# Performance work log

Measured on AMD Instinct MI355X. Metric: run time of the kernel, lower is better.

Reference implementation:

```python
import jax, jax.numpy as jnp
import numpy as np

EPS = 1e-12

def _prelu(x, a):
    return jnp.where(x >= 0, x, a * x)

def _l2norm(x):
    n = jnp.sqrt(jnp.sum(x * x, axis=1, keepdims=True))
    return x / jnp.maximum(n, EPS)

def setup_inputs() -> dict:
    key = jax.random.key(0)
    ks = jax.random.split(key, 8)
    N, E, F_IN, F_OUT = 262144, 4194304, 128, 64
    feat = jax.random.normal(ks[0], (N, F_IN), dtype=jnp.float32)
    edge_src = jax.random.randint(ks[1], (E,), 0, N, dtype=jnp.int32)
    edge_dst = jax.random.randint(ks[2], (E,), 0, N, dtype=jnp.int32)
    edge_w = jax.random.uniform(ks[3], (E,), dtype=jnp.float32)
    # Glorot-uniform projection weight, zero biases (reset_parameters)
    lim = float(np.sqrt(6.0 / (F_IN + F_OUT)))
    weight = jax.random.uniform(ks[4], (F_IN, F_OUT), minval=-lim, maxval=lim, dtype=jnp.float32)
    bias = jnp.zeros((F_OUT,), dtype=jnp.float32)
    prelu_a = jnp.full((1,), 0.25, dtype=jnp.float32)
    lim2 = float(np.sqrt(1.0 / F_OUT))  # torch Linear default init range
    w_sub = jax.random.uniform(ks[5], (F_OUT, F_OUT), minval=-lim2, maxval=lim2, dtype=jnp.float32)
    b_sub = jnp.zeros((F_OUT,), dtype=jnp.float32)
    w_gcn = jax.random.uniform(ks[6], (F_OUT, F_OUT), minval=-lim2, maxval=lim2, dtype=jnp.float32)
    b_gcn = jnp.zeros((F_OUT,), dtype=jnp.float32)
    return {"feat": feat, "edge_src": edge_src, "edge_dst": edge_dst, "edge_w": edge_w,
            "weight": weight, "bias": bias, "prelu_a": prelu_a,
            "w_sub": w_sub, "b_sub": b_sub, "w_gcn": w_gcn, "b_gcn": b_gcn}

def reference(feat, edge_src, edge_dst, edge_w, weight, bias, prelu_a,
              w_sub, b_sub, w_gcn, b_gcn):
    N = feat.shape[0]
    G = N // 4  # 4 nodes per subgraph, anchors at stride 4
    # anchor rows extracted, then zeroed in the feature matrix (in-place in torch)
    anchor_embs = feat[::4, :]
    feat_z = feat.at[::4, :].set(0.0)
    anchor_out = _prelu(anchor_embs @ weight + bias, prelu_a)
    # GraphConv(norm='none', weight=False, bias=False) with edge weights:
    # h[dst] = sum_e w_e * (feat_z @ W)[src_e]
    in_feat = feat_z @ weight                      # [N, F_OUT]
    msgs = in_feat[edge_src] * edge_w[:, None]     # [E, F_OUT]
    h = jax.ops.segment_sum(msgs, edge_dst, num_segments=N)
    h = _prelu(h + bias, prelu_a)
    # AvgPooling per graph (each graph has exactly 4 nodes)
    seg = jnp.arange(N, dtype=jnp.int32) // 4
    subgraph_pool_emb = jax.ops.segment_sum(h, seg, num_segments=G) / 4.0
    gcn_emb = h[::4, :]
    subgraph_pool_emb = subgraph_pool_emb @ w_sub.T + b_sub
    gcn_emb = gcn_emb @ w_gcn.T + b_gcn
    return (_l2norm(subgraph_pool_emb), _l2norm(anchor_out), _l2norm(gcn_emb))
```

## Files before the change

### kernel.cpp

```cpp
#include <hip/hip_runtime.h>
#include <hip/hip_fp16.h>

#define EPSN 1e-12f
#define NBC  256
#define RBF  1024
#define CHK  8192
#define NWGMAX 1024
#define PU   4
#define WQS  16384.0f

typedef _Float16 half8_t __attribute__((ext_vector_type(8)));
typedef float    f32x4  __attribute__((ext_vector_type(4)));

__device__ __forceinline__ float rdlane(float v, int k) {
    return __int_as_float(__builtin_amdgcn_readlane(__float_as_int(v), k));
}
__device__ __forceinline__ float preluf(float x, float a) {
    return x >= 0.0f ? x : a * x;
}

__device__ __forceinline__ void transform_body(
    const float* __restrict__ feat, const float* __restrict__ weight,
    const float* __restrict__ bias, const float* __restrict__ prelu_a,
    __half* __restrict__ in_feat, float* __restrict__ out_anchor,
    int N, int wid, int totalWaves)
{
    const int lane = threadIdx.x & 63;
    const int r    = lane & 15;
    const int g    = lane >> 4;
    const int nt4  = N >> 4;

    half8_t bfr[4][4];
    #pragma unroll
    for (int nt = 0; nt < 4; ++nt)
        #pragma unroll
        for (int kq = 0; kq < 4; ++kq)
            #pragma unroll
            for (int e = 0; e < 8; ++e)
                bfr[nt][kq][e] =
                    (_Float16)weight[(kq * 32 + g * 8 + e) * 64 + nt * 16 + r];

    float bj[4];
    #pragma unroll
    for (int nt = 0; nt < 4; ++nt) bj[nt] = bias[nt * 16 + r];
    const float a = prelu_a[0];

    for (int t = wid; t < nt4; t += totalWaves) {
        const int rb = t << 4;

        f32x4 acc[4];
        #pragma unroll
        for (int nt = 0; nt < 4; ++nt) acc[nt] = (f32x4){0.f, 0.f, 0.f, 0.f};

        const float* fr = feat + (size_t)(rb + r) * 128 + g * 8;
        #pragma unroll
        for (int kq = 0; kq < 4; ++kq) {
            const float4 f0 = *(const float4*)(fr + kq * 32);
            const float4 f1 = *(const float4*)(fr + kq * 32 + 4);
            half8_t af;
            af[0] = (_Float16)f0.x; af[1] = (_Float16)f0.y;
            af[2] = (_Float16)f0.z; af[3] = (_Float16)f0.w;
            af[4] = (_Float16)f1.x; af[5] = (_Float16)f1.y;
            af[6] = (_Float16)f1.z; af[7] = (_Float16)f1.w;
            #pragma unroll
            for (int nt = 0; nt < 4; ++nt)
                acc[nt] = __builtin_amdgcn_mfma_f32_16x16x32_f16(
                    af, bfr[nt][kq], acc[nt], 0, 0, 0);
        }

        const int row0 = rb + g * 4;
        float ss = 0.0f, y[4];
        #pragma unroll
        for (int nt = 0; nt < 4; ++nt) {
            y[nt] = preluf(acc[nt][0] + bj[nt], a);
            ss = fmaf(y[nt], y[nt], ss);
        }
        ss += __shfl_xor(ss, 1, 16);
        ss += __shfl_xor(ss, 2, 16);
        ss += __shfl_xor(ss, 4, 16);
        ss += __shfl_xor(ss, 8, 16);
        const float inv = 1.0f / fmaxf(sqrtf(ss), EPSN);
        #pragma unroll
        for (int nt = 0; nt < 4; ++nt)
            out_anchor[(size_t)(row0 >> 2) * 64 + nt * 16 + r] = y[nt] * inv;
        #pragma unroll
        for (int nt = 0; nt < 4; ++nt)
            in_feat[(size_t)row0 * 64 + nt * 16 + r] = __float2half(0.0f);
        #pragma unroll
        for (int reg = 1; reg < 4; ++reg)
            #pragma unroll
            for (int nt = 0; nt < 4; ++nt)
                in_feat[(size_t)(row0 + reg) * 64 + nt * 16 + r] =
                    __float2half(acc[nt][reg]);
    }
}

__global__ __launch_bounds__(256) void k_tc(
    const float* __restrict__ feat, const float* __restrict__ weight,
    const float* __restrict__ bias, const float* __restrict__ prelu_a,
    __half* __restrict__ in_feat, float* __restrict__ out_anchor, int N,
    int nwg, int twT,
    const int* __restrict__ esrc, const int* __restrict__ edst, int E,
    unsigned* __restrict__ C)
{
    __shared__ unsigned hist[NBC];
    const int t = threadIdx.x;
    if ((int)blockIdx.x >= nwg) {
        const int tIdx = (int)blockIdx.x - nwg;
        const int wid  = tIdx * 4 + (t >> 6);
        transform_body(feat, weight, bias, prelu_a, in_feat, out_anchor,
                       N, wid, twT);
        return;
    }
    const int blk = (int)blockIdx.x;
    hist[t] = 0;
    __syncthreads();
    const int base = blk * CHK;
    for (int r = 0; r < CHK / (16 * 256); ++r) {
        int d[16];
        #pragma unroll
        for (int i = 0; i < 16; ++i) {
            const int idx = base + (r * 16 + i) * 256 + t;
            d[i] = -1;
            if (idx < E) {
                const int s = esrc[idx];
                if ((s & 3) != 0) d[i] = edst[idx];
            }
        }
        #pragma unroll
        for (int i = 0; i < 16; ++i)
            if (d[i] >= 0) atomicAdd(&hist[((unsigned)d[i]) >> 10], 1u);
    }
    __syncthreads();
    C[(size_t)blk * NBC + t] = hist[t];
}

__global__ __launch_bounds__(256) void s_scanA(
    unsigned* __restrict__ C, unsigned* __restrict__ T, int nwg)
{
    __shared__ unsigned ssum[256];
    const int i = blockIdx.x;
    const int t = threadIdx.x;
    const int PER = (nwg + 255) / 256;
    unsigned vals[4];
    unsigned run = 0;
    for (int p = 0; p < PER; ++p) {
        const int blk = t * PER + p;
        const unsigned v = (blk < nwg) ? C[(size_t)blk * NBC + i] : 0u;
        vals[p] = run;
        run += v;
    }
    ssum[t] = run;
    __syncthreads();
    for (int off = 1; off < 256; off <<= 1) {
        unsigned x = (t >= off) ? ssum[t - off] : 0u;
        __syncthreads();
        ssum[t] += x;
        __syncthreads();
    }
    const unsigned texcl = ssum[t] - run;
    for (int p = 0; p < PER; ++p) {
        const int blk = t * PER + p;
        if (blk < nwg) C[(size_t)blk * NBC + i] = texcl + vals[p];
    }
    if (t == 255) T[i] = ssum[255];
}

__global__ __launch_bounds__(1024) void s_scatter4(
    const int* __restrict__ esrc, const int* __restrict__ edst,
    const float* __restrict__ ew, int E,
    const unsigned* __restrict__ C, const unsigned* __restrict__ T, int nwg,
    uint2* __restrict__ recs)
{
    __shared__ uint2    buf[CHK];
    __shared__ unsigned cur[NBC];
    __shared__ unsigned cb [NBC];
    __shared__ unsigned ssum[NBC];
    const int blk = blockIdx.x;
    const int t   = threadIdx.x;

    unsigned Tt = 0, own = 0, nxt = 0;
    if (t < NBC) {
        Tt  = T[t];
        own = C[(size_t)blk * NBC + t];
        nxt = (blk + 1 < nwg) ? C[(size_t)(blk + 1) * NBC + t] : Tt;
        ssum[t] = Tt;
    }
    __syncthreads();
    for (int off = 1; off < NBC; off <<= 1) {
        unsigned x = 0;
        if (t < NBC && t >= off) x = ssum[t - off];
        __syncthreads();
        if (t < NBC) ssum[t] += x;
        __syncthreads();
    }
    const unsigned basepl = (t < NBC) ? (ssum[t] - Tt) : 0u;
    __syncthreads();

    const unsigned myc = nxt - own;
    if (t < NBC) ssum[t] = myc;
    __syncthreads();
    for (int off = 1; off < NBC; off <<= 1) {
        unsigned x = 0;
        if (t < NBC && t >= off) x = ssum[t - off];
        __syncthreads();
        if (t < NBC) ssum[t] += x;
        __syncthreads();
    }
    if (t < NBC) {
        const unsigned excl = ssum[t] - myc;
        cur[t] = excl;
        cb[t]  = basepl + own - excl;
    }
    __syncthreads();
    const unsigned cnt = ssum[NBC - 1];

    const int base = blk * CHK;
    int s8[8], d8[8]; float w8[8];
    #pragma unroll
    for (int i = 0; i < 8; ++i) {
        const int idx = base + i * 1024 + t;
        const bool ok = (idx < E);
        s8[i] = ok ? esrc[idx] : 0;
        d8[i] = ok ? edst[idx] : 0;
        w8[i] = ok ? ew[idx]   : 0.0f;
        if (!ok || (s8[i] & 3) == 0) d8[i] = -1;
    }
    #pragma unroll
    for (int i = 0; i < 8; ++i) {
        if (d8[i] >= 0) {
            const unsigned slot = atomicAdd(&cur[((unsigned)d8[i]) >> 10], 1u);
            const unsigned wq = min((unsigned)(w8[i] * WQS + 0.5f), 16383u);
            buf[slot] = make_uint2(((unsigned)s8[i]) | (wq << 18),
                                   (unsigned)d8[i]);
        }
    }
    __syncthreads();
    for (unsigned i = t; i < cnt; i += 1024) {
        const uint2 rr = buf[i];
        recs[cb[rr.y >> 10] + i] = rr;
    }
}

__global__ __launch_bounds__(1024) void s_sortfine(
    const uint2* __restrict__ recs, const unsigned* __restrict__ T,
    unsigned* __restrict__ recf, unsigned* __restrict__ rs, int N)
{
    __shared__ unsigned hist[RBF];
    __shared__ unsigned sc[RBF];
    __shared__ unsigned bs[NBC];
    const int t = threadIdx.x;
    const int b = blockIdx.x;

    const unsigned Tb = T[b];
    if (t < NBC) bs[t] = T[t];
    __syncthreads();
    for (int off = 1; off < NBC; off <<= 1) {
        unsigned x = 0;
        if (t < NBC && t >= off) x = bs[t - off];
        __syncthreads();
        if (t < NBC) bs[t] += x;
        __syncthreads();
    }
    const unsigned end   = bs[b];
    const unsigned start = end - Tb;
    if (b == NBC - 1 && t == 0) rs[N] = bs[NBC - 1];
    __syncthreads();

    hist[t] = 0;
    __syncthreads();
    for (unsigned i = start + t; i < end; i += 1024)
        atomicAdd(&hist[recs[i].y & (RBF - 1u)], 1u);
    __syncthreads();
    const unsigned my = hist[t];
    sc[t] = my;
    __syncthreads();
    for (int off = 1; off < RBF; off <<= 1) {
        unsigned x = (t >= off) ? sc[t - off] : 0u;
        __syncthreads();
        sc[t] += x;
        __syncthreads();
    }
    const unsigned rowstart = start + sc[t] - my;
    hist[t] = rowstart;
    rs[b * RBF + t] = rowstart;
    __syncthreads();
    for (unsigned i = start + t; i < end; i += 1024) {
        const uint2 r = recs[i];
        const unsigned slot = atomicAdd(&hist[r.y & (RBF - 1u)], 1u);
        recf[slot] = r.x;
    }
}

__global__ __launch_bounds__(256) void s_accum5(
    const __half* __restrict__ in_feat, const unsigned* __restrict__ recf,
    const unsigned* __restrict__ rs, float* __restrict__ h,
    int NROWS, int totalWaves)
{
    const char* ifb  = (const char*)in_feat;
    const int   lane = threadIdx.x & 63;
    const int   l32  = lane & 31;
    const int   hsel = lane >> 5;
    const unsigned colb = (unsigned)l32 * 4u;
    const int wid = (int)((blockIdx.x * (size_t)blockDim.x + threadIdx.x) >> 6);

    for (int row = wid; row < NROWS; row += totalWaves) {
        const unsigned s = rs[row], e = rs[row + 1];
        float acc0 = 0.0f, acc1 = 0.0f;
        for (unsigned done = s; done < e; done += 64u) {
            const int c = (int)min(64u, e - done);
            unsigned rcd = 0u;
            if (lane < c) rcd = recf[done + lane];
            const int pairs = (c + 1) >> 1;
            for (int p0 = 0; p0 < pairs; p0 += PU) {
                unsigned px[PU];
                __half2  hh[PU];
                float    wj[PU];
                #pragma unroll
                for (int pp = 0; pp < PU; ++pp) {
                    const int jv = (p0 + pp) * 2 + hsel;
                    px[pp] = (unsigned)__shfl((int)rcd, jv, 64);
                }
                #pragma unroll
                for (int pp = 0; pp < PU; ++pp) {
                    const unsigned voff =
                        ((px[pp] & 0x3FFFFu) << 7) + colb;
                    hh[pp] = *(const __half2*)(ifb + (size_t)voff);
                    wj[pp] = (float)(px[pp] >> 18);
                }
                #pragma unroll
                for (int pp = 0; pp < PU; ++pp) {
                    acc0 = fmaf(__half2float(__low2half(hh[pp])),  wj[pp], acc0);
                    acc1 = fmaf(__half2float(__high2half(hh[pp])), wj[pp], acc1);
                }
            }
        }
        acc0 += __shfl_xor(acc0, 32, 64);
        acc1 += __shfl_xor(acc1, 32, 64);
        if (hsel == 0) {
            float2 o;
            o.x = acc0 * (1.0f / WQS);
            o.y = acc1 * (1.0f / WQS);
            *(float2*)(h + ((size_t)row << 6) + 2 * l32) = o;
        }
    }
}

__global__ __launch_bounds__(256) void k_transform2(
    const float* __restrict__ feat, const float* __restrict__ weight,
    const float* __restrict__ bias, const float* __restrict__ prelu_a,
    __half* __restrict__ in_feat, float* __restrict__ out_anchor,
    int N, int totalWaves)
{
    const int lane  = threadIdx.x & 63;
    const int wid   = (int)((blockIdx.x * (size_t)blockDim.x + threadIdx.x) >> 6);
    const int tiles = (N + 63) >> 6;

    for (int tile = wid; tile < tiles; tile += totalWaves) {
        const int row = tile * 64 + lane;
        if (row >= N) continue;

        float acc[64];
        #pragma unroll
        for (int j = 0; j < 64; ++j) acc[j] = 0.0f;

        const float4* fp = (const float4*)(feat + (size_t)row * 128);
        #pragma unroll 4
        for (int kc = 0; kc < 32; ++kc) {
            const float4 f = fp[kc];
            const float fs[4] = {f.x, f.y, f.z, f.w};
            #pragma unroll
            for (int kk = 0; kk < 4; ++kk) {
                const float fv = fs[kk];
                const float* wr = weight + (kc * 4 + kk) * 64;
                #pragma unroll
                for (int j = 0; j < 64; ++j)
                    acc[j] = fmaf(fv, wr[j], acc[j]);
            }
        }

        if ((row & 3) == 0) {
            const float a = prelu_a[0];
            float ss = 0.0f;
            #pragma unroll
            for (int j = 0; j < 64; ++j) {
                acc[j] = preluf(acc[j] + bias[j], a);
                ss = fmaf(acc[j], acc[j], ss);
            }
            const float inv = 1.0f / fmaxf(sqrtf(ss), EPSN);
            float* ap = out_anchor + (size_t)(row >> 2) * 64;
            #pragma unroll
            for (int j = 0; j < 64; ++j) ap[j] = acc[j] * inv;
            #pragma unroll
            for (int j = 0; j < 64; ++j)
                in_feat[(size_t)row * 64 + j] = __float2half(0.0f);
        } else {
            #pragma unroll
            for (int j = 0; j < 64; ++j)
                in_feat[(size_t)row * 64 + j] = __float2half(acc[j]);
        }
    }
}

#define K2_U 8
__global__ __launch_bounds__(256) void k_edges(
    const __half* __restrict__ in_feat, const int* __restrict__ esrc,
    const int* __restrict__ edst, const float* __restrict__ ew,
    float* __restrict__ h, int E, int totalWaves)
{
    const int lane = threadIdx.x & 63;
    int wid = (int)((blockIdx.x * (size_t)blockDim.x + threadIdx.x) >> 6);
    wid = __builtin_amdgcn_readfirstlane(wid);
    const int chunk = (E + totalWaves - 1) / totalWaves;
    int e0 = wid * chunk;
    int e1 = min(e0 + chunk, E);
    for (int base = e0; base < e1; base += K2_U) {
        const int nb = min(K2_U, e1 - base);
        int s[K2_U], d[K2_U]; float w[K2_U];
        #pragma unroll
        for (int j = 0; j < K2_U; ++j) {
            int idx = base + ((j < nb) ? j : 0);
            s[j] = esrc[idx]; d[j] = edst[idx]; w[j] = ew[idx];
        }
        float v[K2_U];
        #pragma unroll
        for (int j = 0; j < K2_U; ++j)
            v[j] = __half2float(in_feat[((size_t)s[j] << 6) + lane]);
        #pragma unroll
        for (int j = 0; j < K2_U; ++j)
            if (j < nb) atomicAdd(h + ((size_t)d[j] << 6) + lane, v[j] * w[j]);
    }
}

__global__ __launch_bounds__(256) void k_finalize(
    const float* __restrict__ h, const float* __restrict__ bias,
    const float* __restrict__ prelu_a,
    const float* __restrict__ w_sub, const float* __restrict__ b_sub,
    const float* __restrict__ w_gcn, const float* __restrict__ b_gcn,
    float* __restrict__ out_sub, float* __restrict__ out_gcn,
    int G, int totalWaves)
{
    const int lane = threadIdx.x & 63;
    const int wid = (int)((blockIdx.x * (size_t)blockDim.x + threadIdx.x) >> 6);

    float wsreg[64], wgreg[64];
    #pragma unroll
    for (int k = 0; k < 64; ++k) wsreg[k] = w_sub[lane * 64 + k];
    #pragma unroll
    for (int k = 0; k < 64; ++k) wgreg[k] = w_gcn[lane * 64 + k];
    const float bj  = bias[lane];
    const float bsj = b_sub[lane];
    const float bgj = b_gcn[lane];
    const float a   = prelu_a[0];

    for (int g = wid; g < G; g += totalWaves) {
        const float* hp = h + (size_t)g * 256;
        float p0 = preluf(hp[lane]       + bj, a);
        float p1 = preluf(hp[64  + lane] + bj, a);
        float p2 = preluf(hp[128 + lane] + bj, a);
        float p3 = preluf(hp[192 + lane] + bj, a);
        float pool = (p0 + p1 + p2 + p3) * 0.25f;
        float gcn  = p0;

        float as = bsj, ag = bgj;
        #pragma unroll
        for (int k = 0; k < 64; ++k) {
            as = fmaf(rdlane(pool, k), wsreg[k], as);
            ag = fmaf(rdlane(gcn,  k), wgreg[k], ag);
        }
        float ss = as * as, sg = ag * ag;
        #pragma unroll
        for (int off = 32; off >= 1; off >>= 1) {
            ss += __shfl_xor(ss, off, 64);
            sg += __shfl_xor(sg, off, 64);
        }
        out_sub[(size_t)g * 64 + lane] = as / fmaxf(sqrtf(ss), EPSN);
        out_gcn[(size_t)g * 64 + lane] = ag / fmaxf(sqrtf(sg), EPSN);
    }
}

extern "C" void kernel_launch(void* const* d_in, const int* in_sizes, int n_in,
                              void* d_out, int out_size, void* d_ws, size_t ws_size,
                              hipStream_t stream)
{
    const float* feat    = (const float*)d_in[0];
    const int*   esrc    = (const int*)  d_in[1];
    const int*   edst    = (const int*)  d_in[2];
    const float* ew      = (const float*)d_in[3];
    const float* weight  = (const float*)d_in[4];
    const float* bias    = (const float*)d_in[5];
    const float* prelu_a = (const float*)d_in[6];
    const float* w_sub   = (const float*)d_in[7];
    const float* b_sub   = (const float*)d_in[8];
    const float* w_gcn   = (const float*)d_in[9];
    const float* b_gcn   = (const float*)d_in[10];

    const int N = in_sizes[0] / 128;
    const int E = in_sizes[1];
    const int G = N / 4;
    const int nwg = (E + CHK - 1) / CHK;

    char* wsb = (char*)d_ws;
    const size_t AH    = (size_t)N * 64 * 2;
    const size_t A     = (size_t)N * 64 * 4;
    const size_t offRf = AH + A;
    const size_t offC  = offRf + (size_t)E * 4;
    const size_t offT  = offC  + (size_t)nwg * NBC * 4;
    const size_t offRs = offT  + (size_t)NBC * 4;
    const size_t ws_need = offRs + (size_t)(N + 1) * 4;

    __half*   in_feat = (__half*)wsb;
    float*    h       = (float*)(wsb + AH);
    uint2*    recs    = (uint2*)(wsb + AH);
    unsigned* recf    = (unsigned*)(wsb + offRf);
    unsigned* C       = (unsigned*)(wsb + offC);
    unsigned* T       = (unsigned*)(wsb + offT);
    unsigned* rs      = (unsigned*)(wsb + offRs);

    float* out        = (float*)d_out;
    float* out_sub    = out;
    float* out_anchor = out + (size_t)G * 64;
    float* out_gcn    = out + (size_t)2 * G * 64;

    const bool sorted_path =
        (N == NBC * RBF) && (nwg <= NWGMAX) && ((size_t)E * 8 <= A) &&
        (ws_size >= ws_need);

    if (sorted_path) {
        {
            const int nbT = 2048, twT = nbT * 4;
            k_tc<<<nwg + nbT, 256, 0, stream>>>(feat, weight, bias, prelu_a,
                                                in_feat, out_anchor, N, nwg, twT,
                                                esrc, edst, E, C);
        }
        s_scanA   <<<NBC, 256, 0, stream>>>(C, T, nwg);
        s_scatter4<<<nwg, 1024, 0, stream>>>(esrc, edst, ew, E, C, T, nwg, recs);
        s_sortfine<<<NBC, 1024, 0, stream>>>(recs, T, recf, rs, N);
        {
            const int blocks = 2048, tw = blocks * 4;
            s_accum5<<<blocks, 256, 0, stream>>>(in_feat, recf, rs, h, N, tw);
        }
        {
            const int blocks = 4096, tw = blocks * 4;
            k_finalize<<<blocks, 256, 0, stream>>>(h, bias, prelu_a, w_sub, b_sub,
                                                   w_gcn, b_gcn, out_sub, out_gcn, G, tw);
        }
    } else if (ws_size >= AH + A) {
        {
            const int blocks = 1024, tw = blocks * 4;
            k_transform2<<<blocks, 256, 0, stream>>>(feat, weight, bias, prelu_a,
                                                     in_feat, out_anchor, N, tw);
        }
        hipMemsetAsync(h, 0, A, stream);
        const int blocks = 2048, tw = blocks * 4;
        k_edges<<<blocks, 256, 0, stream>>>(in_feat, esrc, edst, ew, h, E, tw);
        const int fblocks = 4096, ftw = fblocks * 4;
        k_finalize<<<fblocks, 256, 0, stream>>>(h, bias, prelu_a, w_sub, b_sub,
                                                w_gcn, b_gcn, out_sub, out_gcn, G, ftw);
    }
}
```

Measured before the change: 462.1 us.

## Stage transform output and weights through LDS; hoist bucket scan into one kernel

The projection kernel now loads the weight matrix once per block, transposed into LDS as fp16, so each lane builds its MFMA B-fragments with vector LDS reads instead of strided global loads. Each wave stages its 16x64 fp16 output tile in LDS and writes it to in_feat as coalesced 16-byte stores. The global bucket-base prefix scan moves into a new single-block kernel, and the per-block scans in the scatter and fine-sort kernels become wave-shuffle scans, removing repeated LDS scans with many barriers. In exchange the transform blocks use more LDS, which may lower occupancy, and a __syncthreads sits inside the transform loop, which depends on every wave doing the same number of iterations.

```diff
diff --git a/kernel.cpp b/kernel.cpp
--- a/kernel.cpp
+++ b/kernel.cpp
@@ -8,9 +8,11 @@
 #define NWGMAX 1024
 #define PU   4
 #define WQS  16384.0f
+#define TP   68
 
 typedef _Float16 half8_t __attribute__((ext_vector_type(8)));
 typedef float    f32x4  __attribute__((ext_vector_type(4)));
+typedef unsigned uint_ma __attribute__((may_alias));
 
 __device__ __forceinline__ float rdlane(float v, int k) {
     return __int_as_float(__builtin_amdgcn_readlane(__float_as_int(v), k));
@@ -19,13 +21,64 @@
     return x >= 0.0f ? x : a * x;
 }
 
-__device__ __forceinline__ void transform_body(
+__global__ __launch_bounds__(256) void k_tc(
     const float* __restrict__ feat, const float* __restrict__ weight,
     const float* __restrict__ bias, const float* __restrict__ prelu_a,
-    __half* __restrict__ in_feat, float* __restrict__ out_anchor,
-    int N, int wid, int totalWaves)
-{
-    const int lane = threadIdx.x & 63;
+    __half* __restrict__ in_feat, float* __restrict__ out_anchor, int N,
+    int nwg, int twT,
+    const int* __restrict__ esrc, const int* __restrict__ edst, int E,
+    unsigned* __restrict__ C)
+{
+    __shared__ unsigned  hist[NBC];
+    __shared__ _Float16  wT[64 * 128];
+    __shared__ _Float16  st[4][16 * TP];
+
+    const int t = threadIdx.x;
+
+    if ((int)blockIdx.x < nwg) {
+        const int blk = (int)blockIdx.x;
+        hist[t] = 0;
+        __syncthreads();
+        const int base = blk * CHK;
+        for (int r = 0; r < CHK / (16 * 256); ++r) {
+            int d[16];
+            #pragma unroll
+            for (int i = 0; i < 16; ++i) {
+                const int idx = base + (r * 16 + i) * 256 + t;
+                d[i] = -1;
+                if (idx < E) {
+                    const int s = esrc[idx];
+                    if ((s & 3) != 0) d[i] = edst[idx];
+                }
+            }
+            #pragma unroll
+            for (int i = 0; i < 16; ++i)
+                if (d[i] >= 0) atomicAdd(&hist[((unsigned)d[i]) >> 10], 1u);
+        }
+        __syncthreads();
+        C[(size_t)blk * NBC + t] = hist[t];
+        return;
+    }
+
+    const int tIdx = (int)blockIdx.x - nwg;
+    {
+        const float4* w4 = (const float4*)weight;
+        #pragma unroll
+        for (int i = 0; i < 8; ++i) {
+            const int idx = i * 256 + t;
+            const float4 f = w4[idx];
+            const int k = (idx * 4) >> 6;
+            const int c = (idx * 4) & 63;
+            wT[(c + 0) * 128 + k] = (_Float16)f.x;
+            wT[(c + 1) * 128 + k] = (_Float16)f.y;
+            wT[(c + 2) * 128 + k] = (_Float16)f.z;
+            wT[(c + 3) * 128 + k] = (_Float16)f.w;
+        }
+    }
+    __syncthreads();
+
+    const int wv   = t >> 6;
+    const int lane = t & 63;
     const int r    = lane & 15;
     const int g    = lane >> 4;
     const int nt4  = N >> 4;
@@ -35,18 +88,20 @@
     for (int nt = 0; nt < 4; ++nt)
         #pragma unroll
         for (int kq = 0; kq < 4; ++kq)
-            #pragma unroll
-            for (int e = 0; e < 8; ++e)
-                bfr[nt][kq][e] =
-                    (_Float16)weight[(kq * 32 + g * 8 + e) * 64 + nt * 16 + r];
+            bfr[nt][kq] =
+                *(const half8_t*)&wT[(nt * 16 + r) * 128 + kq * 32 + g * 8];
 
     float bj[4];
     #pragma unroll
     for (int nt = 0; nt < 4; ++nt) bj[nt] = bias[nt * 16 + r];
     const float a = prelu_a[0];
 
-    for (int t = wid; t < nt4; t += totalWaves) {
-        const int rb = t << 4;
+    _Float16* stw = &st[wv][0];
+    const int rrow = lane >> 2;
+    const int q    = lane & 3;
+
+    for (int tt = tIdx * 4 + wv; tt < nt4; tt += twT) {
+        const int rb = tt << 4;
 
         f32x4 acc[4];
         #pragma unroll
@@ -83,56 +138,27 @@
         #pragma unroll
         for (int nt = 0; nt < 4; ++nt)
             out_anchor[(size_t)(row0 >> 2) * 64 + nt * 16 + r] = y[nt] * inv;
+
+        const int lr0 = g * 4;
         #pragma unroll
         for (int nt = 0; nt < 4; ++nt)
-            in_feat[(size_t)row0 * 64 + nt * 16 + r] = __float2half(0.0f);
+            stw[lr0 * TP + nt * 16 + r] = (_Float16)0.0f;
         #pragma unroll
         for (int reg = 1; reg < 4; ++reg)
             #pragma unroll
             for (int nt = 0; nt < 4; ++nt)
-                in_feat[(size_t)(row0 + reg) * 64 + nt * 16 + r] =
-                    __float2half(acc[nt][reg]);
-    }
-}
-
-__global__ __launch_bounds__(256) void k_tc(
-    const float* __restrict__ feat, const float* __restrict__ weight,
-    const float* __restrict__ bias, const float* __restrict__ prelu_a,
-    __half* __restrict__ in_feat, float* __restrict__ out_anchor, int N,
-    int nwg, int twT,
-    const int* __restrict__ esrc, const int* __restrict__ edst, int E,
-    unsigned* __restrict__ C)
-{
-    __shared__ unsigned hist[NBC];
-    const int t = threadIdx.x;
-    if ((int)blockIdx.x >= nwg) {
-        const int tIdx = (int)blockIdx.x - nwg;
-        const int wid  = tIdx * 4 + (t >> 6);
-        transform_body(feat, weight, bias, prelu_a, in_feat, out_anchor,
-                       N, wid, twT);
-        return;
-    }
-    const int blk = (int)blockIdx.x;
-    hist[t] = 0;
-    __syncthreads();
-    const int base = blk * CHK;
-    for (int r = 0; r < CHK / (16 * 256); ++r) {
-        int d[16];
-        #pragma unroll
-        for (int i = 0; i < 16; ++i) {
-            const int idx = base + (r * 16 + i) * 256 + t;
-            d[i] = -1;
-            if (idx < E) {
-                const int s = esrc[idx];
-                if ((s & 3) != 0) d[i] = edst[idx];
-            }
-        }
-        #pragma unroll
-        for (int i = 0; i < 16; ++i)
-            if (d[i] >= 0) atomicAdd(&hist[((unsigned)d[i]) >> 10], 1u);
-    }
-    __syncthreads();
-    C[(size_t)blk * NBC + t] = hist[t];
+                stw[(lr0 + reg) * TP + nt * 16 + r] = (_Float16)acc[nt][reg];
+
+        __syncthreads();
+
+        const uint_ma* rp32 = (const uint_ma*)&stw[rrow * TP + q * 16];
+        unsigned v[8];
+        #pragma unroll
+        for (int i = 0; i < 8; ++i) v[i] = rp32[i];
+        uint4* dst = (uint4*)(in_feat + (size_t)(rb + rrow) * 64 + q * 16);
+        dst[0] = make_uint4(v[0], v[1], v[2], v[3]);
+        dst[1] = make_uint4(v[4], v[5], v[6], v[7]);
+    }
 }
 
 __global__ __launch_bounds__(256) void s_scanA(
@@ -166,54 +192,69 @@
     if (t == 255) T[i] = ssum[255];
 }
 
+__global__ __launch_bounds__(256) void s_bases(
+    const unsigned* __restrict__ T, unsigned* __restrict__ basep,
+    unsigned* __restrict__ rs, int N)
+{
+    __shared__ unsigned sc[NBC];
+    const int t = threadIdx.x;
+    const unsigned my = T[t];
+    sc[t] = my;
+    __syncthreads();
+    for (int off = 1; off < NBC; off <<= 1) {
+        unsigned x = (t >= off) ? sc[t - off] : 0u;
+        __syncthreads();
+        sc[t] += x;
+        __syncthreads();
+    }
+    basep[t] = sc[t] - my;
+    if (t == NBC - 1) { basep[NBC] = sc[t]; rs[N] = sc[t]; }
+}
+
 __global__ __launch_bounds__(1024) void s_scatter4(
     const int* __restrict__ esrc, const int* __restrict__ edst,
     const float* __restrict__ ew, int E,
-    const unsigned* __restrict__ C, const unsigned* __restrict__ T, int nwg,
+    const unsigned* __restrict__ C, const unsigned* __restrict__ T,
+    const unsigned* __restrict__ basep, int nwg,
     uint2* __restrict__ recs)
 {
     __shared__ uint2    buf[CHK];
     __shared__ unsigned cur[NBC];
     __shared__ unsigned cb [NBC];
-    __shared__ unsigned ssum[NBC];
+    __shared__ unsigned cntS;
     const int blk = blockIdx.x;
     const int t   = threadIdx.x;
 
-    unsigned Tt = 0, own = 0, nxt = 0;
-    if (t < NBC) {
-        Tt  = T[t];
-        own = C[(size_t)blk * NBC + t];
-        nxt = (blk + 1 < nwg) ? C[(size_t)(blk + 1) * NBC + t] : Tt;
-        ssum[t] = Tt;
-    }
-    __syncthreads();
-    for (int off = 1; off < NBC; off <<= 1) {
-        unsigned x = 0;
-        if (t < NBC && t >= off) x = ssum[t - off];
-        __syncthreads();
-        if (t < NBC) ssum[t] += x;
-        __syncthreads();
-    }
-    const unsigned basepl = (t < NBC) ? (ssum[t] - Tt) : 0u;
-    __syncthreads();
-
-    const unsigned myc = nxt - own;
-    if (t < NBC) ssum[t] = myc;
-    __syncthreads();
-    for (int off = 1; off < NBC; off <<= 1) {
-        unsigned x = 0;
-        if (t < NBC && t >= off) x = ssum[t - off];
-        __syncthreads();
-        if (t < NBC) ssum[t] += x;
-        __syncthreads();
-    }
-    if (t < NBC) {
-        const unsigned excl = ssum[t] - myc;
-        cur[t] = excl;
-        cb[t]  = basepl + own - excl;
-    }
-    __syncthreads();
-    const unsigned cnt = ssum[NBC - 1];
+    if (t < 64) {
+        unsigned vals[4], ownv[4], run = 0;
+        #pragma unroll
+        for (int p = 0; p < 4; ++p) {
+            const int b = t * 4 + p;
+            const unsigned own = C[(size_t)blk * NBC + b];
+            const unsigned nxt =
+                (blk + 1 < nwg) ? C[(size_t)(blk + 1) * NBC + b] : T[b];
+            ownv[p] = own;
+            vals[p] = run;
+            run += nxt - own;
+        }
+        unsigned inc = run;
+        #pragma unroll
+        for (int off = 1; off < 64; off <<= 1) {
+            const unsigned x = __shfl_up(inc, off, 64);
+            if (t >= off) inc += x;
+        }
+        const unsigned lexcl = inc - run;
+        #pragma unroll
+        for (int p = 0; p < 4; ++p) {
+            const int b = t * 4 + p;
+            const unsigned excl = lexcl + vals[p];
+            cur[b] = excl;
+            cb[b]  = basep[b] + ownv[p] - excl;
+        }
+        if (t == 63) cntS = inc;
+    }
+    __syncthreads();
+    const unsigned cnt = cntS;
 
     const int base = blk * CHK;
     int s8[8], d8[8]; float w8[8];
@@ -243,45 +284,41 @@
 }
 
 __global__ __launch_bounds__(1024) void s_sortfine(
-    const uint2* __restrict__ recs, const unsigned* __restrict__ T,
-    unsigned* __restrict__ recf, unsigned* __restrict__ rs, int N)
+    const uint2* __restrict__ recs, const unsigned* __restrict__ basep,
+    unsigned* __restrict__ recf, unsigned* __restrict__ rs)
 {
     __shared__ unsigned hist[RBF];
-    __shared__ unsigned sc[RBF];
-    __shared__ unsigned bs[NBC];
-    const int t = threadIdx.x;
-    const int b = blockIdx.x;
-
-    const unsigned Tb = T[b];
-    if (t < NBC) bs[t] = T[t];
-    __syncthreads();
-    for (int off = 1; off < NBC; off <<= 1) {
-        unsigned x = 0;
-        if (t < NBC && t >= off) x = bs[t - off];
-        __syncthreads();
-        if (t < NBC) bs[t] += x;
-        __syncthreads();
-    }
-    const unsigned end   = bs[b];
-    const unsigned start = end - Tb;
-    if (b == NBC - 1 && t == 0) rs[N] = bs[NBC - 1];
-    __syncthreads();
+    __shared__ unsigned wsum[16];
+    const int t    = threadIdx.x;
+    const int b    = blockIdx.x;
+    const int lane = t & 63;
+    const int wv   = t >> 6;
+
+    const unsigned start = basep[b], end = basep[b + 1];
 
     hist[t] = 0;
     __syncthreads();
     for (unsigned i = start + t; i < end; i += 1024)
         atomicAdd(&hist[recs[i].y & (RBF - 1u)], 1u);
     __syncthreads();
+
     const unsigned my = hist[t];
-    sc[t] = my;
-    __syncthreads();
-    for (int off = 1; off < RBF; off <<= 1) {
-        unsigned x = (t >= off) ? sc[t - off] : 0u;
-        __syncthreads();
-        sc[t] += x;
-        __syncthreads();
-    }
-    const unsigned rowstart = start + sc[t] - my;
+    unsigned inc = my;
+    #pragma unroll
+    for (int off = 1; off < 64; off <<= 1) {
+        const unsigned x = __shfl_up(inc, off, 64);
+        if (lane >= off) inc += x;
+    }
+    if (lane == 63) wsum[wv] = inc;
+    __syncthreads();
+    if (t == 0) {
+        unsigned r = 0;
+        #pragma unroll
+        for (int i = 0; i < 16; ++i) { const unsigned v = wsum[i]; wsum[i] = r; r += v; }
+    }
+    __syncthreads();
+    const unsigned rowstart = start + wsum[wv] + inc - my;
+    __syncthreads();
     hist[t] = rowstart;
     rs[b * RBF + t] = rowstart;
     __syncthreads();
@@ -323,8 +360,7 @@
                 }
                 #pragma unroll
                 for (int pp = 0; pp < PU; ++pp) {
-                    const unsigned voff =
-                        ((px[pp] & 0x3FFFFu) << 7) + colb;
+                    const unsigned voff = ((px[pp] & 0x3FFFFu) << 7) + colb;
                     hh[pp] = *(const __half2*)(ifb + (size_t)voff);
                     wj[pp] = (float)(px[pp] >> 18);
                 }
@@ -506,7 +542,8 @@
     const size_t offRf = AH + A;
     const size_t offC  = offRf + (size_t)E * 4;
     const size_t offT  = offC  + (size_t)nwg * NBC * 4;
-    const size_t offRs = offT  + (size_t)NBC * 4;
+    const size_t offBp = offT  + (size_t)NBC * 4;
+    const size_t offRs = offBp + (size_t)(NBC + 1) * 4;
     const size_t ws_need = offRs + (size_t)(N + 1) * 4;
 
     __half*   in_feat = (__half*)wsb;
@@ -515,6 +552,7 @@
     unsigned* recf    = (unsigned*)(wsb + offRf);
     unsigned* C       = (unsigned*)(wsb + offC);
     unsigned* T       = (unsigned*)(wsb + offT);
+    unsigned* basep   = (unsigned*)(wsb + offBp);
     unsigned* rs      = (unsigned*)(wsb + offRs);
 
     float* out        = (float*)d_out;
@@ -534,8 +572,10 @@
                                                 esrc, edst, E, C);
         }
         s_scanA   <<<NBC, 256, 0, stream>>>(C, T, nwg);
-        s_scatter4<<<nwg, 1024, 0, stream>>>(esrc, edst, ew, E, C, T, nwg, recs);
-        s_sortfine<<<NBC, 1024, 0, stream>>>(recs, T, recf, rs, N);
+        s_bases   <<<1, 256, 0, stream>>>(T, basep, rs, N);
+        s_scatter4<<<nwg, 1024, 0, stream>>>(esrc, edst, ew, E, C, T, basep,
+                                             nwg, recs);
+        s_sortfine<<<NBC, 1024, 0, stream>>>(recs, basep, recf, rs);
         {
             const int blocks = 2048, tw = blocks * 4;
             s_accum5<<<blocks, 256, 0, stream>>>(in_feat, recf, rs, h, N, tw);
```

Result: faster. 445.1 us (-3.7%).
